# Optimization experiments

Measured on AMD Instinct MI355X. Metric: run time of the kernel, lower is better.

Reference implementation:

```python
import jax, jax.numpy as jnp
import numpy as np

N_NODES = 50000
N_EDGES = 800000
N_FEAT, N_HID, N_LATENT = 512, 256, 128


def spmm(rows, cols, vals, dense):
    # out[r] += vals[e] * dense[cols[e]]  -- COO SpMM via segment_sum
    gathered = dense[cols] * vals[:, None]          # [E, d]
    return jax.ops.segment_sum(gathered, rows, num_segments=N_NODES)


def setup_inputs() -> dict:
    key = jax.random.key(0)
    ks = jax.random.split(key, 8)
    x = jax.random.normal(ks[0], (N_NODES, N_FEAT), dtype=jnp.float32)
    edge_rows = jax.random.randint(ks[1], (N_EDGES,), 0, N_NODES, dtype=jnp.int32)
    edge_cols = jax.random.randint(ks[2], (N_EDGES,), 0, N_NODES, dtype=jnp.int32)
    edge_vals = jax.random.uniform(ks[3], (N_EDGES,), dtype=jnp.float32)
    # Glorot-style init like the torch GraphConvolution
    W1 = jax.random.normal(ks[4], (N_FEAT, N_HID), dtype=jnp.float32) / np.sqrt(N_FEAT)
    b1 = jnp.zeros((N_HID,), dtype=jnp.float32)
    W2 = jax.random.normal(ks[5], (N_HID, N_LATENT), dtype=jnp.float32) / np.sqrt(N_HID)
    b2 = jnp.zeros((N_LATENT,), dtype=jnp.float32)
    return {"x": x, "edge_rows": edge_rows, "edge_cols": edge_cols,
            "edge_vals": edge_vals, "W1": W1, "b1": b1, "W2": W2, "b2": b2}


def reference(x, edge_rows, edge_cols, edge_vals, W1, b1, W2, b2):
    # layer 1: relu(adj @ (x @ W1) + b1)
    h = spmm(edge_rows, edge_cols, edge_vals, x @ W1) + b1
    h = jax.nn.relu(h)
    # layer 2: relu(adj @ (h @ W2) + b2)
    z = spmm(edge_rows, edge_cols, edge_vals, h @ W2) + b2
    return jax.nn.relu(z)
```

## Files before the change

kernel.cpp:

```cpp
#include <hip/hip_runtime.h>
#include <hip/hip_bf16.h>


typedef __attribute__((ext_vector_type(8))) short bf16x8;
typedef __attribute__((ext_vector_type(8))) unsigned short ushort8;
typedef __attribute__((ext_vector_type(4))) float f32x4;

#define NN 50000
#define NE 800000
#define NF 512
#define NH 256
#define NL 128
#define NB ((NN + 255) / 256)

static __device__ __forceinline__ unsigned short f2bf(float f) {
  union { float f; unsigned int u; } v; v.f = f;
  unsigned int r = v.u + 0x7fffu + ((v.u >> 16) & 1u);
  return (unsigned short)(r >> 16);
}
static __device__ __forceinline__ float bf2f(unsigned short u) {
  union { unsigned int u; float f; } v; v.u = (unsigned int)u << 16;
  return v.f;
}

static __device__ __forceinline__ unsigned int pkbf(float lo, float hi) {
  unsigned int r;
  asm("v_cvt_pk_bf16_f32 %0, %1, %2" : "=v"(r) : "v"(lo), "v"(hi));
  return r;
}
static __device__ __forceinline__ uint4 pk8(float4 a, float4 b) {
  uint4 o;
  o.x = pkbf(a.x, a.y); o.y = pkbf(a.z, a.w);
  o.z = pkbf(b.x, b.y); o.w = pkbf(b.z, b.w);
  return o;
}

static __device__ __forceinline__ void gll16(const void* g, void* l) {
  __builtin_amdgcn_global_load_lds(
      (const __attribute__((address_space(1))) void*)g,
      (__attribute__((address_space(3))) void*)l, 16, 0, 0);
}

extern "C" __global__ void k_hist(const int* __restrict__ rows, int* __restrict__ counts, int n) {
  int i = blockIdx.x * 256 + threadIdx.x;
  if (i < n) atomicAdd(&counts[rows[i]], 1);
}

extern "C" __global__ __launch_bounds__(256) void k_blocksum(
    const int* __restrict__ counts, int* __restrict__ bsum, int n) {
  __shared__ int s[256];
  int t = threadIdx.x;
  int i = blockIdx.x * 256 + t;
  s[t] = (i < n) ? counts[i] : 0;
  __syncthreads();
  for (int off = 128; off > 0; off >>= 1) {
    if (t < off) s[t] += s[t + off];
    __syncthreads();
  }
  if (t == 0) bsum[blockIdx.x] = s[0];
}

extern "C" __global__ __launch_bounds__(256) void k_scansums(
    const int* __restrict__ bsum, int* __restrict__ bpre, int* __restrict__ rp, int nb, int n) {
  __shared__ int s[256];
  int t = threadIdx.x;
  int v = (t < nb) ? bsum[t] : 0;
  s[t] = v;
  __syncthreads();
  for (int off = 1; off < 256; off <<= 1) {
    int u = (t >= off) ? s[t - off] : 0;
    __syncthreads();
    s[t] += u;
    __syncthreads();
  }
  if (t < nb) bpre[t] = s[t] - v;
  if (t == 255) rp[n] = s[255];
}

extern "C" __global__ __launch_bounds__(256) void k_scanfin(
    const int* __restrict__ counts, const int* __restrict__ bpre,
    int* __restrict__ rp, int* __restrict__ cur, int n) {
  __shared__ int s[256];
  int t = threadIdx.x;
  int i = blockIdx.x * 256 + t;
  int c = (i < n) ? counts[i] : 0;
  s[t] = c;
  __syncthreads();
  for (int off = 1; off < 256; off <<= 1) {
    int u = (t >= off) ? s[t - off] : 0;
    __syncthreads();
    s[t] += u;
    __syncthreads();
  }
  if (i < n) {
    int e = bpre[blockIdx.x] + s[t] - c;
    rp[i] = e;
    cur[i] = e;
  }
}

extern "C" __global__ void k_scatter(const int* __restrict__ rows, const int* __restrict__ cols,
    const float* __restrict__ vals, int* __restrict__ cur, int2* __restrict__ ep, int n) {
  int i = blockIdx.x * 256 + threadIdx.x;
  if (i < n) {
    int p = atomicAdd(&cur[rows[i]], 1);
    int2 e; e.x = cols[i]; e.y = __float_as_int(vals[i]);
    ep[p] = e;
  }
}

extern "C" __global__ void k_transcast(const float* __restrict__ w, unsigned short* __restrict__ wt,
                                       int K, int N) {
  int k = blockIdx.x; int n = threadIdx.x;
  wt[(size_t)n * K + k] = f2bf(w[(size_t)k * N + n]);
}

extern "C" __global__ __launch_bounds__(256) void k_gemm1(
    const float* __restrict__ A, const unsigned short* __restrict__ BT,
    unsigned short* __restrict__ C) {
  __shared__ __align__(16) unsigned short sA[2][64 * 64];
  __shared__ __align__(16) unsigned short sB[2][128 * 64];
  int tid = threadIdx.x;
  int lane = tid & 63, wid = tid >> 6;
  int wm = (wid >> 1) * 32, wn = (wid & 1) * 64;
  int bm = blockIdx.x * 64, bn = blockIdx.y * 128;
  int l15 = lane & 15, lq = lane >> 4;
  int swzbase = l15 & 7;
  f32x4 acc[2][4];
#pragma unroll
  for (int i = 0; i < 2; ++i)
#pragma unroll
    for (int j = 0; j < 4; ++j) acc[i][j] = (f32x4){0.f, 0.f, 0.f, 0.f};

  float4 ra[2][2];

#pragma unroll
  for (int j = 0; j < 2; ++j) {
    int u = tid + 256 * j;
    int row = u >> 3, cu = u & 7;
    int ga = bm + row; if (ga >= NN) ga = NN - 1;
    const float* src = A + (size_t)ga * NF + cu * 8;
    ra[j][0] = ((const float4*)src)[0];
    ra[j][1] = ((const float4*)src)[1];
  }
#pragma unroll
  for (int j = 0; j < 4; ++j) {
    int u = tid + 256 * j;
    int row = u >> 3, cu = u & 7;
    int g = cu ^ (row & 7);
    gll16(BT + (size_t)(bn + row) * NF + g * 8, &sB[0][u * 8]);
  }
#pragma unroll
  for (int j = 0; j < 2; ++j) {
    int u = tid + 256 * j;
    int row = u >> 3, cu = u & 7;
    *(uint4*)(&sA[0][row * 64 + (cu ^ (row & 7)) * 8]) = pk8(ra[j][0], ra[j][1]);
  }
  __syncthreads();

  int cur = 0;
  for (int t = 0; t < NF / 64; ++t) {
    int k1 = (t + 1) * 64;
    if (t < NF / 64 - 1) {
#pragma unroll
      for (int j = 0; j < 2; ++j) {
        int u = tid + 256 * j;
        int row = u >> 3, cu = u & 7;
        int ga = bm + row; if (ga >= NN) ga = NN - 1;
        const float* src = A + (size_t)ga * NF + k1 + cu * 8;
        ra[j][0] = ((const float4*)src)[0];
        ra[j][1] = ((const float4*)src)[1];
      }
#pragma unroll
      for (int j = 0; j < 4; ++j) {
        int u = tid + 256 * j;
        int row = u >> 3, cu = u & 7;
        int g = cu ^ (row & 7);
        gll16(BT + (size_t)(bn + row) * NF + k1 + g * 8, &sB[cur ^ 1][u * 8]);
      }
    }
#pragma unroll
    for (int ks = 0; ks < 64; ks += 32) {
      bf16x8 af[2], bfr[4];
#pragma unroll
      for (int tt = 0; tt < 2; ++tt) {
        int sz = (((ks >> 3) + lq) ^ swzbase) * 8;
        af[tt] = *(const bf16x8*)(&sA[cur][(wm + tt * 16 + l15) * 64 + sz]);
      }
#pragma unroll
      for (int tt = 0; tt < 4; ++tt) {
        int sz = (((ks >> 3) + lq) ^ swzbase) * 8;
        bfr[tt] = *(const bf16x8*)(&sB[cur][(wn + tt * 16 + l15) * 64 + sz]);
      }
#pragma unroll
      for (int mt = 0; mt < 2; ++mt)
#pragma unroll
        for (int nt = 0; nt < 4; ++nt)
          acc[mt][nt] = __builtin_amdgcn_mfma_f32_16x16x32_bf16(af[mt], bfr[nt], acc[mt][nt], 0, 0, 0);
    }
    if (t < NF / 64 - 1) {
#pragma unroll
      for (int j = 0; j < 2; ++j) {
        int u = tid + 256 * j;
        int row = u >> 3, cu = u & 7;
        *(uint4*)(&sA[cur ^ 1][row * 64 + (cu ^ (row & 7)) * 8]) = pk8(ra[j][0], ra[j][1]);
      }
    }
    __syncthreads();
    cur ^= 1;
  }
#pragma unroll
  for (int mt = 0; mt < 2; ++mt) {
#pragma unroll
    for (int r = 0; r < 4; ++r) {
      int gr = bm + wm + mt * 16 + lq * 4 + r;
      if (gr < NN) {
#pragma unroll
        for (int nt = 0; nt < 4; ++nt) {
          int gc = bn + wn + nt * 16 + l15;
          C[(size_t)gr * NH + gc] = f2bf(acc[mt][nt][r]);
        }
      }
    }
  }
}

extern "C" __global__ __launch_bounds__(256) void k_gemm2(
    const unsigned short* __restrict__ A, const unsigned short* __restrict__ BT,
    unsigned short* __restrict__ C) {
  __shared__ __align__(16) unsigned short sA[2][64 * 64];
  __shared__ __align__(16) unsigned short sB[2][128 * 64];
  int tid = threadIdx.x;
  int lane = tid & 63, wid = tid >> 6;
  int wm = (wid >> 1) * 32, wn = (wid & 1) * 64;
  int bm = blockIdx.x * 64;
  int l15 = lane & 15, lq = lane >> 4;
  int swzbase = l15 & 7;
  f32x4 acc[2][4];
#pragma unroll
  for (int i = 0; i < 2; ++i)
#pragma unroll
    for (int j = 0; j < 4; ++j) acc[i][j] = (f32x4){0.f, 0.f, 0.f, 0.f};

#pragma unroll
  for (int j = 0; j < 2; ++j) {
    int u = tid + 256 * j;
    int row = u >> 3, cu = u & 7;
    int ga = bm + row; if (ga >= NN) ga = NN - 1;
    int g = cu ^ (row & 7);
    gll16(A + (size_t)ga * NH + g * 8, &sA[0][u * 8]);
  }
#pragma unroll
  for (int j = 0; j < 4; ++j) {
    int u = tid + 256 * j;
    int row = u >> 3, cu = u & 7;
    int g = cu ^ (row & 7);
    gll16(BT + (size_t)row * NH + g * 8, &sB[0][u * 8]);
  }
  __syncthreads();

  int cur = 0;
  for (int t = 0; t < NH / 64; ++t) {
    int k1 = (t + 1) * 64;
    if (t < NH / 64 - 1) {
#pragma unroll
      for (int j = 0; j < 2; ++j) {
        int u = tid + 256 * j;
        int row = u >> 3, cu = u & 7;
        int ga = bm + row; if (ga >= NN) ga = NN - 1;
        int g = cu ^ (row & 7);
        gll16(A + (size_t)ga * NH + k1 + g * 8, &sA[cur ^ 1][u * 8]);
      }
#pragma unroll
      for (int j = 0; j < 4; ++j) {
        int u = tid + 256 * j;
        int row = u >> 3, cu = u & 7;
        int g = cu ^ (row & 7);
        gll16(BT + (size_t)row * NH + k1 + g * 8, &sB[cur ^ 1][u * 8]);
      }
    }
#pragma unroll
    for (int ks = 0; ks < 64; ks += 32) {
      bf16x8 af[2], bfr[4];
#pragma unroll
      for (int tt = 0; tt < 2; ++tt)
        af[tt] = *(const bf16x8*)(&sA[cur][(wm + tt * 16 + l15) * 64 + (((ks >> 3) + lq) ^ swzbase) * 8]);
#pragma unroll
      for (int tt = 0; tt < 4; ++tt)
        bfr[tt] = *(const bf16x8*)(&sB[cur][(wn + tt * 16 + l15) * 64 + (((ks >> 3) + lq) ^ swzbase) * 8]);
#pragma unroll
      for (int mt = 0; mt < 2; ++mt)
#pragma unroll
        for (int nt = 0; nt < 4; ++nt)
          acc[mt][nt] = __builtin_amdgcn_mfma_f32_16x16x32_bf16(af[mt], bfr[nt], acc[mt][nt], 0, 0, 0);
    }
    __syncthreads();
    cur ^= 1;
  }
#pragma unroll
  for (int mt = 0; mt < 2; ++mt) {
#pragma unroll
    for (int r = 0; r < 4; ++r) {
      int gr = bm + wm + mt * 16 + lq * 4 + r;
      if (gr < NN) {
#pragma unroll
        for (int nt = 0; nt < 4; ++nt) {
          int gc = wn + nt * 16 + l15;
          C[(size_t)gr * NL + gc] = f2bf(acc[mt][nt][r]);
        }
      }
    }
  }
}

extern "C" __global__ __launch_bounds__(256) void k_spmm256(
    const int* __restrict__ rp, const int2* __restrict__ ep,
    const unsigned short* __restrict__ src, const float* __restrict__ bias,
    ushort4* __restrict__ out) {
  int row = blockIdx.x * 4 + (threadIdx.x >> 6);
  int lane = threadIdx.x & 63;
  if (row >= NN) return;
  int e0 = __builtin_amdgcn_readfirstlane(rp[row]);
  int e1 = __builtin_amdgcn_readfirstlane(rp[row + 1]);
  const ushort4* srcv = (const ushort4*)src;
  float4 acc = {0.f, 0.f, 0.f, 0.f};
  int e = e0;
  for (; e + 8 <= e1; e += 8) {
    int2 p[8]; ushort4 g[8];
#pragma unroll
    for (int j = 0; j < 8; ++j) p[j] = ep[e + j];
#pragma unroll
    for (int j = 0; j < 8; ++j) g[j] = srcv[(size_t)p[j].x * (NH / 4) + lane];
#pragma unroll
    for (int j = 0; j < 8; ++j) {
      float v = __int_as_float(p[j].y);
      acc.x = fmaf(v, bf2f(g[j].x), acc.x); acc.y = fmaf(v, bf2f(g[j].y), acc.y);
      acc.z = fmaf(v, bf2f(g[j].z), acc.z); acc.w = fmaf(v, bf2f(g[j].w), acc.w);
    }
  }
  for (; e + 4 <= e1; e += 4) {
    int2 p[4]; ushort4 g[4];
#pragma unroll
    for (int j = 0; j < 4; ++j) p[j] = ep[e + j];
#pragma unroll
    for (int j = 0; j < 4; ++j) g[j] = srcv[(size_t)p[j].x * (NH / 4) + lane];
#pragma unroll
    for (int j = 0; j < 4; ++j) {
      float v = __int_as_float(p[j].y);
      acc.x = fmaf(v, bf2f(g[j].x), acc.x); acc.y = fmaf(v, bf2f(g[j].y), acc.y);
      acc.z = fmaf(v, bf2f(g[j].z), acc.z); acc.w = fmaf(v, bf2f(g[j].w), acc.w);
    }
  }
  for (; e < e1; ++e) {
    int2 p = ep[e];
    float v = __int_as_float(p.y);
    ushort4 g = srcv[(size_t)p.x * (NH / 4) + lane];
    acc.x = fmaf(v, bf2f(g.x), acc.x); acc.y = fmaf(v, bf2f(g.y), acc.y);
    acc.z = fmaf(v, bf2f(g.z), acc.z); acc.w = fmaf(v, bf2f(g.w), acc.w);
  }
  float4 b = ((const float4*)bias)[lane];
  ushort4 o;
  o.x = f2bf(fmaxf(acc.x + b.x, 0.f));
  o.y = f2bf(fmaxf(acc.y + b.y, 0.f));
  o.z = f2bf(fmaxf(acc.z + b.z, 0.f));
  o.w = f2bf(fmaxf(acc.w + b.w, 0.f));
  out[(size_t)row * (NH / 4) + lane] = o;
}

extern "C" __global__ __launch_bounds__(256) void k_spmm128(
    const int* __restrict__ rp, const int2* __restrict__ ep,
    const unsigned short* __restrict__ src, const float* __restrict__ bias,
    float2* __restrict__ out) {
  int row = blockIdx.x * 4 + (threadIdx.x >> 6);
  int lane = threadIdx.x & 63;
  if (row >= NN) return;
  int e0 = __builtin_amdgcn_readfirstlane(rp[row]);
  int e1 = __builtin_amdgcn_readfirstlane(rp[row + 1]);
  const ushort2* srcv = (const ushort2*)src;
  float2 acc = {0.f, 0.f};
  int e = e0;
  for (; e + 8 <= e1; e += 8) {
    int2 p[8]; ushort2 g[8];
#pragma unroll
    for (int j = 0; j < 8; ++j) p[j] = ep[e + j];
#pragma unroll
    for (int j = 0; j < 8; ++j) g[j] = srcv[(size_t)p[j].x * (NL / 2) + lane];
#pragma unroll
    for (int j = 0; j < 8; ++j) {
      float v = __int_as_float(p[j].y);
      acc.x = fmaf(v, bf2f(g[j].x), acc.x); acc.y = fmaf(v, bf2f(g[j].y), acc.y);
    }
  }
  for (; e + 4 <= e1; e += 4) {
    int2 p[4]; ushort2 g[4];
#pragma unroll
    for (int j = 0; j < 4; ++j) p[j] = ep[e + j];
#pragma unroll
    for (int j = 0; j < 4; ++j) g[j] = srcv[(size_t)p[j].x * (NL / 2) + lane];
#pragma unroll
    for (int j = 0; j < 4; ++j) {
      float v = __int_as_float(p[j].y);
      acc.x = fmaf(v, bf2f(g[j].x), acc.x); acc.y = fmaf(v, bf2f(g[j].y), acc.y);
    }
  }
  for (; e < e1; ++e) {
    int2 p = ep[e];
    float v = __int_as_float(p.y);
    ushort2 g = srcv[(size_t)p.x * (NL / 2) + lane];
    acc.x = fmaf(v, bf2f(g.x), acc.x); acc.y = fmaf(v, bf2f(g.y), acc.y);
  }
  float2 b = ((const float2*)bias)[lane];
  float2 o;
  o.x = fmaxf(acc.x + b.x, 0.f);
  o.y = fmaxf(acc.y + b.y, 0.f);
  out[(size_t)row * (NL / 2) + lane] = o;
}

extern "C" void kernel_launch(void* const* d_in, const int* in_sizes, int n_in,
                              void* d_out, int out_size, void* d_ws, size_t ws_size,
                              hipStream_t stream) {
  const float* x   = (const float*)d_in[0];
  const int* erow  = (const int*)d_in[1];
  const int* ecol  = (const int*)d_in[2];
  const float* ev  = (const float*)d_in[3];
  const float* W1  = (const float*)d_in[4];
  const float* b1  = (const float*)d_in[5];
  const float* W2  = (const float*)d_in[6];
  const float* b2  = (const float*)d_in[7];

  char* ws = (char*)d_ws;
  unsigned short* xwb = (unsigned short*)(ws + 0);
  unsigned short* hbf = (unsigned short*)(ws + 25600000);
  unsigned short* hwb = (unsigned short*)(ws + 51200000);
  unsigned short* w1t = (unsigned short*)(ws + 64000000);
  unsigned short* w2t = (unsigned short*)(ws + 64262144);
  int* rp    = (int*)(ws + 64327680);
  int* cur   = (int*)(ws + 64528384);
  int* cnt   = (int*)(ws + 64729088);
  int* bsum  = (int*)(ws + 64929792);
  int* bpre  = (int*)(ws + 64930816);
  int2* ep   = (int2*)(ws + 64931840);

  hipMemsetAsync(cnt, 0, NN * sizeof(int), stream);
  k_hist<<<NE / 256, 256, 0, stream>>>(erow, cnt, NE);
  k_blocksum<<<NB, 256, 0, stream>>>(cnt, bsum, NN);
  k_scansums<<<1, 256, 0, stream>>>(bsum, bpre, rp, NB, NN);
  k_scanfin<<<NB, 256, 0, stream>>>(cnt, bpre, rp, cur, NN);
  k_scatter<<<NE / 256, 256, 0, stream>>>(erow, ecol, ev, cur, ep, NE);

  k_transcast<<<NF, NH, 0, stream>>>(W1, w1t, NF, NH);
  k_gemm1<<<dim3((NN + 63) / 64, NH / 128), 256, 0, stream>>>(x, w1t, xwb);
  k_spmm256<<<NN / 4, 256, 0, stream>>>(rp, ep, xwb, b1, (ushort4*)hbf);

  k_transcast<<<NH, NL, 0, stream>>>(W2, w2t, NH, NL);
  k_gemm2<<<(NN + 63) / 64, 256, 0, stream>>>(hbf, w2t, hwb);
  k_spmm128<<<NN / 4, 256, 0, stream>>>(rp, ep, hwb, b2, (float2*)d_out);
}
```

Before: 380.5 us.

## Deepen gemm1 prefetch pipeline with explicit vmcnt waits and raw barriers

Restructures the first GEMM's K loop into a fully unrolled software pipeline. A tiles are prefetched two steps ahead in a double register set, and B tiles one step ahead via direct global-to-LDS loads. Syncthreads is replaced by explicit s_waitcnt vmcnt/lgkmcnt counts, scheduling fences and s_barrier, so global loads can stay in flight across compute. The aim is to hide global-load latency of the fp32 A operand. The cost is more registers and fragile hand-tuned wait counts that must match the exact number of issued loads.

```diff
diff --git a/kernel.cpp b/kernel.cpp
--- a/kernel.cpp
+++ b/kernel.cpp
@@ -12,6 +12,11 @@
 #define NH 256
 #define NL 128
 #define NB ((NN + 255) / 256)
+
+#define WAIT_VM(N) asm volatile("s_waitcnt vmcnt(" #N ")" ::: "memory")
+#define WAIT_VM_LGKM(N) asm volatile("s_waitcnt vmcnt(" #N ") lgkmcnt(0)" ::: "memory")
+#define SCHED_FENCE() __builtin_amdgcn_sched_barrier(0)
+#define BARRIER() __builtin_amdgcn_s_barrier()
 
 static __device__ __forceinline__ unsigned short f2bf(float f) {
   union { float f; unsigned int u; } v; v.f = f;
@@ -132,65 +137,49 @@
 #pragma unroll
     for (int j = 0; j < 4; ++j) acc[i][j] = (f32x4){0.f, 0.f, 0.f, 0.f};
 
-  float4 ra[2][2];
-
-#pragma unroll
-  for (int j = 0; j < 2; ++j) {
-    int u = tid + 256 * j;
-    int row = u >> 3, cu = u & 7;
-    int ga = bm + row; if (ga >= NN) ga = NN - 1;
-    const float* src = A + (size_t)ga * NF + cu * 8;
-    ra[j][0] = ((const float4*)src)[0];
-    ra[j][1] = ((const float4*)src)[1];
-  }
-#pragma unroll
-  for (int j = 0; j < 4; ++j) {
-    int u = tid + 256 * j;
-    int row = u >> 3, cu = u & 7;
-    int g = cu ^ (row & 7);
-    gll16(BT + (size_t)(bn + row) * NF + g * 8, &sB[0][u * 8]);
-  }
-#pragma unroll
-  for (int j = 0; j < 2; ++j) {
-    int u = tid + 256 * j;
-    int row = u >> 3, cu = u & 7;
-    *(uint4*)(&sA[0][row * 64 + (cu ^ (row & 7)) * 8]) = pk8(ra[j][0], ra[j][1]);
-  }
-  __syncthreads();
-
-  int cur = 0;
-  for (int t = 0; t < NF / 64; ++t) {
-    int k1 = (t + 1) * 64;
-    if (t < NF / 64 - 1) {
-#pragma unroll
-      for (int j = 0; j < 2; ++j) {
-        int u = tid + 256 * j;
-        int row = u >> 3, cu = u & 7;
-        int ga = bm + row; if (ga >= NN) ga = NN - 1;
-        const float* src = A + (size_t)ga * NF + k1 + cu * 8;
-        ra[j][0] = ((const float4*)src)[0];
-        ra[j][1] = ((const float4*)src)[1];
-      }
-#pragma unroll
-      for (int j = 0; j < 4; ++j) {
-        int u = tid + 256 * j;
-        int row = u >> 3, cu = u & 7;
-        int g = cu ^ (row & 7);
-        gll16(BT + (size_t)(bn + row) * NF + k1 + g * 8, &sB[cur ^ 1][u * 8]);
-      }
-    }
+  float4 ra[2][2][2];
+
+  auto loadA = [&](int t, int set) {
+#pragma unroll
+    for (int j = 0; j < 2; ++j) {
+      int u = tid + 256 * j;
+      int row = u >> 3, cu = u & 7;
+      int ga = bm + row; if (ga >= NN) ga = NN - 1;
+      const float* src = A + (size_t)ga * NF + t * 64 + cu * 8;
+      ra[set][j][0] = ((const float4*)src)[0];
+      ra[set][j][1] = ((const float4*)src)[1];
+    }
+  };
+  auto issueB = [&](int t) {
+#pragma unroll
+    for (int j = 0; j < 4; ++j) {
+      int u = tid + 256 * j;
+      int row = u >> 3, cu = u & 7;
+      int g = cu ^ (row & 7);
+      gll16(BT + (size_t)(bn + row) * NF + t * 64 + g * 8, &sB[t & 1][u * 8]);
+    }
+  };
+  auto writeA = [&](int t, int set) {
+#pragma unroll
+    for (int j = 0; j < 2; ++j) {
+      int u = tid + 256 * j;
+      int row = u >> 3, cu = u & 7;
+      *(uint4*)(&sA[t & 1][row * 64 + (cu ^ (row & 7)) * 8]) = pk8(ra[set][j][0], ra[set][j][1]);
+    }
+  };
+  auto comp = [&](int t) {
 #pragma unroll
     for (int ks = 0; ks < 64; ks += 32) {
       bf16x8 af[2], bfr[4];
 #pragma unroll
       for (int tt = 0; tt < 2; ++tt) {
         int sz = (((ks >> 3) + lq) ^ swzbase) * 8;
-        af[tt] = *(const bf16x8*)(&sA[cur][(wm + tt * 16 + l15) * 64 + sz]);
+        af[tt] = *(const bf16x8*)(&sA[t & 1][(wm + tt * 16 + l15) * 64 + sz]);
       }
 #pragma unroll
       for (int tt = 0; tt < 4; ++tt) {
         int sz = (((ks >> 3) + lq) ^ swzbase) * 8;
-        bfr[tt] = *(const bf16x8*)(&sB[cur][(wn + tt * 16 + l15) * 64 + sz]);
+        bfr[tt] = *(const bf16x8*)(&sB[t & 1][(wn + tt * 16 + l15) * 64 + sz]);
       }
 #pragma unroll
       for (int mt = 0; mt < 2; ++mt)
@@ -198,17 +187,39 @@
         for (int nt = 0; nt < 4; ++nt)
           acc[mt][nt] = __builtin_amdgcn_mfma_f32_16x16x32_bf16(af[mt], bfr[nt], acc[mt][nt], 0, 0, 0);
     }
-    if (t < NF / 64 - 1) {
-#pragma unroll
-      for (int j = 0; j < 2; ++j) {
-        int u = tid + 256 * j;
-        int row = u >> 3, cu = u & 7;
-        *(uint4*)(&sA[cur ^ 1][row * 64 + (cu ^ (row & 7)) * 8]) = pk8(ra[j][0], ra[j][1]);
-      }
-    }
-    __syncthreads();
-    cur ^= 1;
-  }
+  };
+
+  loadA(0, 0);
+  SCHED_FENCE();
+  issueB(0);
+  issueB(1);
+  SCHED_FENCE();
+  WAIT_VM(8);
+  writeA(0, 0);
+  SCHED_FENCE();
+  loadA(1, 1);
+  SCHED_FENCE();
+  WAIT_VM_LGKM(8);
+  SCHED_FENCE();
+  BARRIER();
+
+#pragma unroll
+  for (int t = 0; t < 8; ++t) {
+    if (t >= 1 && t <= 6) { issueB(t + 1); SCHED_FENCE(); }
+    if (t <= 5) { loadA(t + 2, t & 1); SCHED_FENCE(); }
+    comp(t);
+    if (t <= 6) {
+      if (t == 0) { WAIT_VM(4); }
+      else if (t == 6) { WAIT_VM(4); }
+      else { WAIT_VM(8); }
+      writeA(t + 1, (t + 1) & 1);
+      SCHED_FENCE();
+      if (t == 6) { WAIT_VM_LGKM(0); } else { WAIT_VM_LGKM(4); }
+      SCHED_FENCE();
+      BARRIER();
+    }
+  }
+
 #pragma unroll
   for (int mt = 0; mt < 2; ++mt) {
 #pragma unroll
```

Measured after the change: 376.1 us. About the same (-1.1%).
